# Performance work log

Hardware: AMD Instinct MI355X
Metric: run time of the kernel (lower is better)

The kernel has to match this reference:

```python
import jax, jax.numpy as jnp
import numpy as np

B, T = 64, 256
IN, HID, OUT = 512, 1024, 256
NUM_DOMAINS = 20

def setup_inputs() -> dict:
    key = jax.random.key(0)
    k1, k2, k3, k4 = jax.random.split(key, 4)
    x = jax.random.normal(k1, (B, T, IN), dtype=jnp.float32)
    hetero_info = jax.random.randint(k2, (B, 2), 0, NUM_DOMAINS, dtype=jnp.int64)
    # embedding tables init N(0, 0.02) as in the torch module
    fc1_table = 0.02 * jax.random.normal(k3, (NUM_DOMAINS, IN * HID + HID), dtype=jnp.float32)
    fc2_table = 0.02 * jax.random.normal(k4, (NUM_DOMAINS, HID * OUT + OUT), dtype=jnp.float32)
    return {"x": x, "hetero_info": hetero_info, "fc1_table": fc1_table, "fc2_table": fc2_table}

def reference(x, hetero_info, fc1_table, fc2_table):
    domain_id = hetero_info[:, 0].astype(jnp.int32)
    Bn = domain_id.shape[0]
    fc1_param = fc1_table[domain_id]                     # (B, IN*HID + HID)
    w1 = fc1_param[:, : IN * HID].reshape(Bn, IN, HID)   # (B, IN, HID)
    b1 = fc1_param[:, IN * HID:].reshape(Bn, 1, HID)
    fc2_param = fc2_table[domain_id]                     # (B, HID*OUT + OUT)
    w2 = fc2_param[:, : HID * OUT].reshape(Bn, HID, OUT) # (B, HID, OUT)
    b2 = fc2_param[:, HID * OUT:].reshape(Bn, 1, OUT)
    h = jnp.einsum('bti,bih->bth', x, w1) + b1
    h = jax.nn.gelu(h, approximate=False)  # torch nn.GELU default = exact erf
    out = jnp.einsum('bth,bho->bto', h, w2) + b2
    return out
```

## Files before the change

kernel.cpp:

```cpp
#include <hip/hip_runtime.h>
#include <math.h>

#define B_  64
#define T_  256
#define IN_ 512
#define HID_ 1024
#define OUT_ 256
#define NDOM 20

typedef __bf16 bf16_t;
typedef __bf16 bf16x8 __attribute__((ext_vector_type(8)));
typedef float  f32x4  __attribute__((ext_vector_type(4)));

__device__ __forceinline__ unsigned f2bf_bits(float f) {
    unsigned u = __builtin_bit_cast(unsigned, f);
    return (u + 0x7FFFu + ((u >> 16) & 1u)) >> 16;
}
__device__ __forceinline__ unsigned pack_bf16x2(float x, float y) {
    return f2bf_bits(x) | (f2bf_bits(y) << 16);
}

__device__ __forceinline__ void gl_lds16(const void* g, void* l) {
    __builtin_amdgcn_global_load_lds(
        (const __attribute__((address_space(1))) unsigned*)g,
        (__attribute__((address_space(3))) unsigned*)l,
        16, 0, 0);
}

__global__ __launch_bounds__(256) void prepass(
    const float* __restrict__ X,  bf16_t* __restrict__ Xbf,
    const float* __restrict__ t1, bf16_t* __restrict__ W1t, float* __restrict__ b1,
    const float* __restrict__ t2, bf16_t* __restrict__ W2t, float* __restrict__ b2)
{
    const int bid = blockIdx.x;
    const int tid = threadIdx.x;

    if (bid < 8192) {
        const size_t idx = (size_t)bid * 256 + tid;
        float4 v = ((const float4*)X)[idx];
        uint2 p;
        p.x = pack_bf16x2(v.x, v.y);
        p.y = pack_bf16x2(v.z, v.w);
        ((uint2*)Xbf)[idx] = p;
        return;
    }

    __shared__ float t[64][65];

    const float* table; bf16_t* Wt; float* Bias;
    int K, N, d, n0, k0;
    if (bid < 10752) {
        const int r = bid - 8192;
        K = IN_; N = HID_;
        d = r >> 7;
        n0 = (r & 15) * 64;
        k0 = ((r >> 4) & 7) * 64;
        table = t1; Wt = W1t; Bias = b1;
    } else {
        const int r = bid - 10752;
        K = HID_; N = OUT_;
        d = r >> 6;
        n0 = (r & 3) * 64;
        k0 = ((r >> 2) & 15) * 64;
        table = t2; Wt = W2t; Bias = b2;
    }

    const float* W = table + (size_t)d * ((size_t)K * N + N);

    #pragma unroll
    for (int r = 0; r < 4; ++r) {
        const int kl = (tid >> 4) + r * 16;
        const int nl = (tid & 15) * 4;
        float4 v = *(const float4*)(W + (size_t)(k0 + kl) * N + n0 + nl);
        t[kl][nl + 0] = v.x; t[kl][nl + 1] = v.y;
        t[kl][nl + 2] = v.z; t[kl][nl + 3] = v.w;
    }
    __syncthreads();

    bf16_t* Wtd = Wt + (size_t)d * K * N;
    #pragma unroll
    for (int r = 0; r < 4; ++r) {
        const int nl = (tid >> 4) + r * 16;
        const int k4 = (tid & 15) * 4;
        uint2 p;
        p.x = pack_bf16x2(t[k4 + 0][nl], t[k4 + 1][nl]);
        p.y = pack_bf16x2(t[k4 + 2][nl], t[k4 + 3][nl]);
        *(uint2*)(Wtd + (size_t)(n0 + nl) * K + k0 + k4) = p;
    }

    if (k0 == 0 && tid < 64)
        Bias[(size_t)d * N + n0 + tid] = W[(size_t)K * N + n0 + tid];
}

#define CT_STRIDE 136
__global__ __launch_bounds__(256) void fc1_gemm(
    const bf16_t* __restrict__ Xbf,
    const bf16_t* __restrict__ W1t,
    const float*  __restrict__ Bias,
    const int*    __restrict__ hetero,
    bf16_t*       __restrict__ H)
{
    const int id   = blockIdx.x;
    const int g    = id & 127;
    const int nidx = id >> 7;
    const int b    = g >> 1;
    const int m0   = (g & 1) * 128;
    const int n0   = nidx * 128;
    const int d    = hetero[2 * b];
    const bf16_t* W    = W1t + (size_t)d * HID_ * IN_;
    const float*  bias = Bias + (size_t)d * HID_;
    const bf16_t* A    = Xbf + (size_t)(b * 256 + m0) * IN_;

    __shared__ __attribute__((aligned(16))) char smem[128 * CT_STRIDE * 2];
    bf16_t* LdsA = (bf16_t*)smem;
    bf16_t* LdsB = (bf16_t*)(smem + 16384);
    bf16_t* Ct   = (bf16_t*)smem;

    const int tid  = threadIdx.x;
    const int wave = tid >> 6;
    const int lane = tid & 63;
    const int l16  = lane & 15;
    const int quad = lane >> 4;
    const int wm   = (wave >> 1) * 64;
    const int wn   = (wave & 1) * 64;

    f32x4 acc[4][4] = {};

    for (int kk = 0; kk < IN_; kk += 64) {
        #pragma unroll
        for (int cc = 0; cc < 4; ++cc) {
            const int r0  = wave * 32 + cc * 8;
            const int row = r0 + (lane >> 3);
            const int cs  = (lane & 7) ^ (row & 7);
            gl_lds16(A + (size_t)row * IN_ + kk + cs * 8, &LdsA[r0 * 64]);
        }
        #pragma unroll
        for (int cc = 0; cc < 4; ++cc) {
            const int r0  = wave * 32 + cc * 8;
            const int row = r0 + (lane >> 3);
            const int cs  = (lane & 7) ^ (row & 7);
            gl_lds16(W + (size_t)(n0 + row) * IN_ + kk + cs * 8, &LdsB[r0 * 64]);
        }
        __syncthreads();

        #pragma unroll
        for (int h = 0; h < 2; ++h) {
            bf16x8 af[4], bfg[4];
            #pragma unroll
            for (int i = 0; i < 4; ++i) {
                const int r = wm + i * 16 + l16;
                const int c = (h * 4 + quad) ^ (r & 7);
                af[i] = *(const bf16x8*)&LdsA[r * 64 + c * 8];
            }
            #pragma unroll
            for (int j = 0; j < 4; ++j) {
                const int r = wn + j * 16 + l16;
                const int c = (h * 4 + quad) ^ (r & 7);
                bfg[j] = *(const bf16x8*)&LdsB[r * 64 + c * 8];
            }
            #pragma unroll
            for (int i = 0; i < 4; ++i)
                #pragma unroll
                for (int j = 0; j < 4; ++j)
                    acc[i][j] = __builtin_amdgcn_mfma_f32_16x16x32_bf16(bfg[j], af[i], acc[i][j], 0, 0, 0);
        }
        __syncthreads();
    }

    #pragma unroll
    for (int i = 0; i < 4; ++i) {
        const int m = wm + i * 16 + l16;
        #pragma unroll
        for (int j = 0; j < 4; ++j) {
            const int nl = wn + j * 16 + quad * 4;
            const float4 b4 = *(const float4*)&bias[n0 + nl];
            float v0 = acc[i][j][0] + b4.x;
            float v1 = acc[i][j][1] + b4.y;
            float v2 = acc[i][j][2] + b4.z;
            float v3 = acc[i][j][3] + b4.w;
            v0 = 0.5f * v0 * (1.0f + erff(v0 * 0.70710678f));
            v1 = 0.5f * v1 * (1.0f + erff(v1 * 0.70710678f));
            v2 = 0.5f * v2 * (1.0f + erff(v2 * 0.70710678f));
            v3 = 0.5f * v3 * (1.0f + erff(v3 * 0.70710678f));
            uint2 p;
            p.x = pack_bf16x2(v0, v1);
            p.y = pack_bf16x2(v2, v3);
            *(uint2*)&Ct[m * CT_STRIDE + nl] = p;
        }
    }
    __syncthreads();

    #pragma unroll
    for (int it = 0; it < 8; ++it) {
        const int row = it * 16 + (tid >> 4);
        const int ch  = tid & 15;
        uint4 v = *(const uint4*)&Ct[row * CT_STRIDE + ch * 8];
        *(uint4*)&H[((size_t)(b * 256 + m0 + row)) * HID_ + n0 + ch * 8] = v;
    }
}

__global__ __launch_bounds__(256) void fc2_gemm(
    const bf16_t* __restrict__ H,
    const bf16_t* __restrict__ W2t,
    const float*  __restrict__ Bias,
    const int*    __restrict__ hetero,
    float*        __restrict__ Out)
{
    const int id   = blockIdx.x;
    const int g    = id & 255;
    const int nidx = id >> 8;
    const int b    = g >> 2;
    const int m0   = (g & 3) * 64;
    const int n0   = nidx * 64;
    const int d    = hetero[2 * b];
    const bf16_t* W    = W2t + (size_t)d * OUT_ * HID_;
    const float*  bias = Bias + (size_t)d * OUT_;

    __shared__ __attribute__((aligned(16))) bf16_t LdsA[64 * 128];
    __shared__ __attribute__((aligned(16))) bf16_t LdsB[64 * 128];

    const int tid  = threadIdx.x;
    const int wave = tid >> 6;
    const int lane = tid & 63;
    const int l16  = lane & 15;
    const int quad = lane >> 4;
    const int wm   = (wave >> 1) * 32;
    const int wn   = (wave & 1) * 32;

    f32x4 acc[2][2] = {};

    for (int kk = 0; kk < HID_; kk += 128) {
        #pragma unroll
        for (int cc = 0; cc < 4; ++cc) {
            const int r0  = wave * 16 + cc * 4;
            const int row = r0 + (lane >> 4);
            const int cs  = (lane & 15) ^ (row & 15);
            gl_lds16(H + (size_t)(b * 256 + m0 + row) * HID_ + kk + cs * 8,
                     &LdsA[r0 * 128]);
        }
        #pragma unroll
        for (int cc = 0; cc < 4; ++cc) {
            const int r0  = wave * 16 + cc * 4;
            const int row = r0 + (lane >> 4);
            const int cs  = (lane & 15) ^ (row & 15);
            gl_lds16(W + (size_t)(n0 + row) * HID_ + kk + cs * 8,
                     &LdsB[r0 * 128]);
        }
        __syncthreads();

        #pragma unroll
        for (int h = 0; h < 4; ++h) {
            bf16x8 af[2], bfg[2];
            #pragma unroll
            for (int i = 0; i < 2; ++i) {
                const int r = wm + i * 16 + l16;
                const int c = (h * 4 + quad) ^ (r & 15);
                af[i] = *(const bf16x8*)&LdsA[r * 128 + c * 8];
            }
            #pragma unroll
            for (int j = 0; j < 2; ++j) {
                const int r = wn + j * 16 + l16;
                const int c = (h * 4 + quad) ^ (r & 15);
                bfg[j] = *(const bf16x8*)&LdsB[r * 128 + c * 8];
            }
            #pragma unroll
            for (int i = 0; i < 2; ++i)
                #pragma unroll
                for (int j = 0; j < 2; ++j)
                    acc[i][j] = __builtin_amdgcn_mfma_f32_16x16x32_bf16(bfg[j], af[i], acc[i][j], 0, 0, 0);
        }
        __syncthreads();
    }

    #pragma unroll
    for (int i = 0; i < 2; ++i) {
        const int m = m0 + wm + i * 16 + l16;
        #pragma unroll
        for (int j = 0; j < 2; ++j) {
            const int nl = wn + j * 16 + quad * 4;
            const float4 b4 = *(const float4*)&bias[n0 + nl];
            float4 o;
            o.x = acc[i][j][0] + b4.x;
            o.y = acc[i][j][1] + b4.y;
            o.z = acc[i][j][2] + b4.z;
            o.w = acc[i][j][3] + b4.w;
            *(float4*)&Out[(size_t)(b * 256 + m) * OUT_ + n0 + nl] = o;
        }
    }
}

extern "C" void kernel_launch(void* const* d_in, const int* in_sizes, int n_in,
                              void* d_out, int out_size, void* d_ws, size_t ws_size,
                              hipStream_t stream) {
    const float* x         = (const float*)d_in[0];
    const int*   hetero    = (const int*)d_in[1];
    const float* fc1_table = (const float*)d_in[2];
    const float* fc2_table = (const float*)d_in[3];
    float*       out       = (float*)d_out;

    char* ws = (char*)d_ws;
    bf16_t* W1t = (bf16_t*)(ws);
    bf16_t* W2t = (bf16_t*)(ws + 20971520);
    float*  b1  = (float*)(ws + 31457280);
    float*  b2  = (float*)(ws + 31539200);
    bf16_t* H   = (bf16_t*)(ws + 31559680);

    bf16_t* Xbf = (bf16_t*)d_out;

    prepass<<<dim3(12032), 256, 0, stream>>>(
        x, Xbf, fc1_table, W1t, b1, fc2_table, W2t, b2);

    fc1_gemm<<<dim3(1024), 256, 0, stream>>>(Xbf, W1t, b1, hetero, H);
    fc2_gemm<<<dim3(1024), 256, 0, stream>>>(H, W2t, b2, hetero, out);
}
```

Before: 189.5 us.

## Load weights directly from global into registers and double-buffer activation tiles

Both GEMMs stop staging the weight tile through LDS. Each wave now reads its B fragments straight from global memory (L2-resident per-domain weights), and only the activation tile is staged, double-buffered so the next chunk's load overlaps the MFMAs. Tile shapes change: fc1 uses 64x256 tiles with the blocks of each batch spread across the grid, and fc2 uses 32x256 full-N tiles in 512 blocks. This removes LDS traffic and one barrier per iteration, but exposes global load latency on the weight fragments and cuts the fc2 grid size.

Result: slower. 211.4 us (+11.5%).

```diff
diff --git a/kernel.cpp b/kernel.cpp
--- a/kernel.cpp
+++ b/kernel.cpp
@@ -92,7 +92,7 @@
         Bias[(size_t)d * N + n0 + tid] = W[(size_t)K * N + n0 + tid];
 }
 
-#define CT_STRIDE 136
+#define CT1_STRIDE 264
 __global__ __launch_bounds__(256) void fc1_gemm(
     const bf16_t* __restrict__ Xbf,
     const bf16_t* __restrict__ W1t,
@@ -101,75 +101,89 @@
     bf16_t*       __restrict__ H)
 {
     const int id   = blockIdx.x;
-    const int g    = id & 127;
-    const int nidx = id >> 7;
-    const int b    = g >> 1;
-    const int m0   = (g & 1) * 128;
-    const int n0   = nidx * 128;
+    const int b    = id & 63;
+    const int rest = id >> 6;
+    const int m0   = (rest & 3) * 64;
+    const int n0   = (rest >> 2) * 256;
     const int d    = hetero[2 * b];
     const bf16_t* W    = W1t + (size_t)d * HID_ * IN_;
     const float*  bias = Bias + (size_t)d * HID_;
     const bf16_t* A    = Xbf + (size_t)(b * 256 + m0) * IN_;
 
-    __shared__ __attribute__((aligned(16))) char smem[128 * CT_STRIDE * 2];
-    bf16_t* LdsA = (bf16_t*)smem;
-    bf16_t* LdsB = (bf16_t*)(smem + 16384);
-    bf16_t* Ct   = (bf16_t*)smem;
+    __shared__ __attribute__((aligned(16))) char smem[64 * CT1_STRIDE * 2];
+    bf16_t* LdsA0 = (bf16_t*)smem;
+    bf16_t* LdsA1 = (bf16_t*)(smem + 8192);
+    bf16_t* Ct    = (bf16_t*)smem;
 
     const int tid  = threadIdx.x;
     const int wave = tid >> 6;
     const int lane = tid & 63;
     const int l16  = lane & 15;
     const int quad = lane >> 4;
-    const int wm   = (wave >> 1) * 64;
-    const int wn   = (wave & 1) * 64;
+    const int wn   = wave * 64;
+
+    const int st_r0a = wave * 16;
+    const int st_row = lane >> 3;
+    const int st_c   = lane & 7;
 
     f32x4 acc[4][4] = {};
 
-    for (int kk = 0; kk < IN_; kk += 64) {
-        #pragma unroll
-        for (int cc = 0; cc < 4; ++cc) {
-            const int r0  = wave * 32 + cc * 8;
-            const int row = r0 + (lane >> 3);
-            const int cs  = (lane & 7) ^ (row & 7);
-            gl_lds16(A + (size_t)row * IN_ + kk + cs * 8, &LdsA[r0 * 64]);
-        }
-        #pragma unroll
-        for (int cc = 0; cc < 4; ++cc) {
-            const int r0  = wave * 32 + cc * 8;
-            const int row = r0 + (lane >> 3);
-            const int cs  = (lane & 7) ^ (row & 7);
-            gl_lds16(W + (size_t)(n0 + row) * IN_ + kk + cs * 8, &LdsB[r0 * 64]);
-        }
+    {
+        bf16_t* dst = LdsA0;
+        #pragma unroll
+        for (int cc = 0; cc < 2; ++cc) {
+            const int r0  = st_r0a + cc * 8;
+            const int row = r0 + st_row;
+            const int cs  = st_c ^ (row & 7);
+            gl_lds16(A + (size_t)row * IN_ + cs * 8, &dst[r0 * 64]);
+        }
+    }
+
+    for (int kki = 0; kki < 8; ++kki) {
+        const int kk = kki * 64;
         __syncthreads();
 
+        bf16_t* cur = (kki & 1) ? LdsA1 : LdsA0;
+        if (kki < 7) {
+            bf16_t* nxt = (kki & 1) ? LdsA0 : LdsA1;
+            #pragma unroll
+            for (int cc = 0; cc < 2; ++cc) {
+                const int r0  = st_r0a + cc * 8;
+                const int row = r0 + st_row;
+                const int cs  = st_c ^ (row & 7);
+                gl_lds16(A + (size_t)row * IN_ + kk + 64 + cs * 8, &nxt[r0 * 64]);
+            }
+        }
+
+        bf16x8 bfg[2][4];
+        #pragma unroll
+        for (int h = 0; h < 2; ++h)
+            #pragma unroll
+            for (int j = 0; j < 4; ++j)
+                bfg[h][j] = *(const bf16x8*)(W +
+                    (size_t)(n0 + wn + j * 16 + l16) * IN_ + kk + h * 32 + quad * 8);
+
         #pragma unroll
         for (int h = 0; h < 2; ++h) {
-            bf16x8 af[4], bfg[4];
+            bf16x8 af[4];
             #pragma unroll
             for (int i = 0; i < 4; ++i) {
-                const int r = wm + i * 16 + l16;
+                const int r = i * 16 + l16;
                 const int c = (h * 4 + quad) ^ (r & 7);
-                af[i] = *(const bf16x8*)&LdsA[r * 64 + c * 8];
-            }
-            #pragma unroll
-            for (int j = 0; j < 4; ++j) {
-                const int r = wn + j * 16 + l16;
-                const int c = (h * 4 + quad) ^ (r & 7);
-                bfg[j] = *(const bf16x8*)&LdsB[r * 64 + c * 8];
+                af[i] = *(const bf16x8*)&cur[r * 64 + c * 8];
             }
             #pragma unroll
             for (int i = 0; i < 4; ++i)
                 #pragma unroll
                 for (int j = 0; j < 4; ++j)
-                    acc[i][j] = __builtin_amdgcn_mfma_f32_16x16x32_bf16(bfg[j], af[i], acc[i][j], 0, 0, 0);
-        }
-        __syncthreads();
-    }
+                    acc[i][j] = __builtin_amdgcn_mfma_f32_16x16x32_bf16(bfg[h][j], af[i], acc[i][j], 0, 0, 0);
+        }
+    }
+    __syncthreads();
 
     #pragma unroll
     for (int i = 0; i < 4; ++i) {
-        const int m = wm + i * 16 + l16;
+        const int m = i * 16 + l16;
         #pragma unroll
         for (int j = 0; j < 4; ++j) {
             const int nl = wn + j * 16 + quad * 4;
@@ -185,16 +199,16 @@
             uint2 p;
             p.x = pack_bf16x2(v0, v1);
             p.y = pack_bf16x2(v2, v3);
-            *(uint2*)&Ct[m * CT_STRIDE + nl] = p;
+            *(uint2*)&Ct[m * CT1_STRIDE + nl] = p;
         }
     }
     __syncthreads();
 
     #pragma unroll
     for (int it = 0; it < 8; ++it) {
-        const int row = it * 16 + (tid >> 4);
-        const int ch  = tid & 15;
-        uint4 v = *(const uint4*)&Ct[row * CT_STRIDE + ch * 8];
+        const int row = it * 8 + (tid >> 5);
+        const int ch  = tid & 31;
+        uint4 v = *(const uint4*)&Ct[row * CT1_STRIDE + ch * 8];
         *(uint4*)&H[((size_t)(b * 256 + m0 + row)) * HID_ + n0 + ch * 8] = v;
     }
 }
@@ -207,84 +221,84 @@
     float*        __restrict__ Out)
 {
     const int id   = blockIdx.x;
-    const int g    = id & 255;
-    const int nidx = id >> 8;
-    const int b    = g >> 2;
-    const int m0   = (g & 3) * 64;
-    const int n0   = nidx * 64;
+    const int b    = id & 63;
+    const int m0   = (id >> 6) * 32;
     const int d    = hetero[2 * b];
     const bf16_t* W    = W2t + (size_t)d * OUT_ * HID_;
     const float*  bias = Bias + (size_t)d * OUT_;
-
-    __shared__ __attribute__((aligned(16))) bf16_t LdsA[64 * 128];
-    __shared__ __attribute__((aligned(16))) bf16_t LdsB[64 * 128];
+    const bf16_t* A    = H + (size_t)(b * 256 + m0) * HID_;
+
+    __shared__ __attribute__((aligned(16))) bf16_t LdsA[2][32 * 64];
 
     const int tid  = threadIdx.x;
     const int wave = tid >> 6;
     const int lane = tid & 63;
     const int l16  = lane & 15;
     const int quad = lane >> 4;
-    const int wm   = (wave >> 1) * 32;
-    const int wn   = (wave & 1) * 32;
-
-    f32x4 acc[2][2] = {};
-
-    for (int kk = 0; kk < HID_; kk += 128) {
-        #pragma unroll
-        for (int cc = 0; cc < 4; ++cc) {
-            const int r0  = wave * 16 + cc * 4;
-            const int row = r0 + (lane >> 4);
-            const int cs  = (lane & 15) ^ (row & 15);
-            gl_lds16(H + (size_t)(b * 256 + m0 + row) * HID_ + kk + cs * 8,
-                     &LdsA[r0 * 128]);
-        }
-        #pragma unroll
-        for (int cc = 0; cc < 4; ++cc) {
-            const int r0  = wave * 16 + cc * 4;
-            const int row = r0 + (lane >> 4);
-            const int cs  = (lane & 15) ^ (row & 15);
-            gl_lds16(W + (size_t)(n0 + row) * HID_ + kk + cs * 8,
-                     &LdsB[r0 * 128]);
-        }
+    const int wn   = wave * 64;
+
+    const int st_r0  = wave * 8;
+    const int st_row = lane >> 3;
+    const int st_c   = lane & 7;
+
+    f32x4 acc[2][4] = {};
+
+    {
+        const int row = st_r0 + st_row;
+        const int cs  = st_c ^ (row & 7);
+        gl_lds16(A + (size_t)row * HID_ + cs * 8, &LdsA[0][st_r0 * 64]);
+    }
+
+    for (int kki = 0; kki < 16; ++kki) {
+        const int kk = kki * 64;
         __syncthreads();
 
-        #pragma unroll
-        for (int h = 0; h < 4; ++h) {
-            bf16x8 af[2], bfg[2];
+        const bf16_t* cur = LdsA[kki & 1];
+        if (kki < 15) {
+            bf16_t* nxt = LdsA[(kki + 1) & 1];
+            const int row = st_r0 + st_row;
+            const int cs  = st_c ^ (row & 7);
+            gl_lds16(A + (size_t)row * HID_ + kk + 64 + cs * 8, &nxt[st_r0 * 64]);
+        }
+
+        bf16x8 bfg[2][4];
+        #pragma unroll
+        for (int h = 0; h < 2; ++h)
+            #pragma unroll
+            for (int j = 0; j < 4; ++j)
+                bfg[h][j] = *(const bf16x8*)(W +
+                    (size_t)(wn + j * 16 + l16) * HID_ + kk + h * 32 + quad * 8);
+
+        #pragma unroll
+        for (int h = 0; h < 2; ++h) {
+            bf16x8 af[2];
             #pragma unroll
             for (int i = 0; i < 2; ++i) {
-                const int r = wm + i * 16 + l16;
-                const int c = (h * 4 + quad) ^ (r & 15);
-                af[i] = *(const bf16x8*)&LdsA[r * 128 + c * 8];
-            }
-            #pragma unroll
-            for (int j = 0; j < 2; ++j) {
-                const int r = wn + j * 16 + l16;
-                const int c = (h * 4 + quad) ^ (r & 15);
-                bfg[j] = *(const bf16x8*)&LdsB[r * 128 + c * 8];
+                const int r = i * 16 + l16;
+                const int c = (h * 4 + quad) ^ (r & 7);
+                af[i] = *(const bf16x8*)&cur[r * 64 + c * 8];
             }
             #pragma unroll
             for (int i = 0; i < 2; ++i)
                 #pragma unroll
-                for (int j = 0; j < 2; ++j)
-                    acc[i][j] = __builtin_amdgcn_mfma_f32_16x16x32_bf16(bfg[j], af[i], acc[i][j], 0, 0, 0);
-        }
-        __syncthreads();
+                for (int j = 0; j < 4; ++j)
+                    acc[i][j] = __builtin_amdgcn_mfma_f32_16x16x32_bf16(bfg[h][j], af[i], acc[i][j], 0, 0, 0);
+        }
     }
 
     #pragma unroll
     for (int i = 0; i < 2; ++i) {
-        const int m = m0 + wm + i * 16 + l16;
-        #pragma unroll
-        for (int j = 0; j < 2; ++j) {
+        const int m = m0 + i * 16 + l16;
+        #pragma unroll
+        for (int j = 0; j < 4; ++j) {
             const int nl = wn + j * 16 + quad * 4;
-            const float4 b4 = *(const float4*)&bias[n0 + nl];
+            const float4 b4 = *(const float4*)&bias[nl];
             float4 o;
             o.x = acc[i][j][0] + b4.x;
             o.y = acc[i][j][1] + b4.y;
             o.z = acc[i][j][2] + b4.z;
             o.w = acc[i][j][3] + b4.w;
-            *(float4*)&Out[(size_t)(b * 256 + m) * OUT_ + n0 + nl] = o;
+            *(float4*)&Out[(size_t)(b * 256 + m) * OUT_ + nl] = o;
         }
     }
 }
@@ -311,5 +325,5 @@
         x, Xbf, fc1_table, W1t, b1, fc2_table, W2t, b2);
 
     fc1_gemm<<<dim3(1024), 256, 0, stream>>>(Xbf, W1t, b1, hetero, H);
-    fc2_gemm<<<dim3(1024), 256, 0, stream>>>(H, W2t, b2, hetero, out);
-}
+    fc2_gemm<<<dim3(512), 256, 0, stream>>>(H, W2t, b2, hetero, out);
+}
```

## Widen fc1 GEMM tile to 128x256 and reorder block-to-batch mapping

Applied to the files above, without the earlier changes.

The fc1 GEMM block tile grows from 128x128 to 128x256, so each wave holds a 64x128 accumulator and the grid is halved to 512 blocks. Block indices now map batch fastest, and the epilogue writes the tile back in two 128-column halves through the shared staging buffer. The aim is to reuse each A tile across more output columns and cut global and LDS loads per MFMA. The cost is roughly double the accumulator registers, which may lower occupancy, and fewer blocks to spread across the CUs.

After: 249.3 us. 1.32x slower.

```diff
diff --git a/kernel.cpp b/kernel.cpp
--- a/kernel.cpp
+++ b/kernel.cpp
@@ -101,17 +101,16 @@
     bf16_t*       __restrict__ H)
 {
     const int id   = blockIdx.x;
-    const int g    = id & 127;
-    const int nidx = id >> 7;
-    const int b    = g >> 1;
-    const int m0   = (g & 1) * 128;
-    const int n0   = nidx * 128;
+    const int b    = id & 63;
+    const int rest = id >> 6;
+    const int m0   = (rest & 1) * 128;
+    const int n0   = (rest >> 1) * 256;
     const int d    = hetero[2 * b];
     const bf16_t* W    = W1t + (size_t)d * HID_ * IN_;
     const float*  bias = Bias + (size_t)d * HID_;
     const bf16_t* A    = Xbf + (size_t)(b * 256 + m0) * IN_;
 
-    __shared__ __attribute__((aligned(16))) char smem[128 * CT_STRIDE * 2];
+    __shared__ __attribute__((aligned(16))) char smem[49152];
     bf16_t* LdsA = (bf16_t*)smem;
     bf16_t* LdsB = (bf16_t*)(smem + 16384);
     bf16_t* Ct   = (bf16_t*)smem;
@@ -122,21 +121,21 @@
     const int l16  = lane & 15;
     const int quad = lane >> 4;
     const int wm   = (wave >> 1) * 64;
-    const int wn   = (wave & 1) * 64;
-
-    f32x4 acc[4][4] = {};
+    const int wn   = (wave & 1) * 128;
+
+    f32x4 acc[4][8] = {};
 
     for (int kk = 0; kk < IN_; kk += 64) {
         #pragma unroll
         for (int cc = 0; cc < 4; ++cc) {
-            const int r0  = wave * 32 + cc * 8;
+            const int r0  = cc * 32 + wave * 8;
             const int row = r0 + (lane >> 3);
             const int cs  = (lane & 7) ^ (row & 7);
             gl_lds16(A + (size_t)row * IN_ + kk + cs * 8, &LdsA[r0 * 64]);
         }
         #pragma unroll
-        for (int cc = 0; cc < 4; ++cc) {
-            const int r0  = wave * 32 + cc * 8;
+        for (int cc = 0; cc < 8; ++cc) {
+            const int r0  = cc * 32 + wave * 8;
             const int row = r0 + (lane >> 3);
             const int cs  = (lane & 7) ^ (row & 7);
             gl_lds16(W + (size_t)(n0 + row) * IN_ + kk + cs * 8, &LdsB[r0 * 64]);
@@ -145,7 +144,7 @@
 
         #pragma unroll
         for (int h = 0; h < 2; ++h) {
-            bf16x8 af[4], bfg[4];
+            bf16x8 af[4], bfg[8];
             #pragma unroll
             for (int i = 0; i < 4; ++i) {
                 const int r = wm + i * 16 + l16;
@@ -153,7 +152,7 @@
                 af[i] = *(const bf16x8*)&LdsA[r * 64 + c * 8];
             }
             #pragma unroll
-            for (int j = 0; j < 4; ++j) {
+            for (int j = 0; j < 8; ++j) {
                 const int r = wn + j * 16 + l16;
                 const int c = (h * 4 + quad) ^ (r & 7);
                 bfg[j] = *(const bf16x8*)&LdsB[r * 64 + c * 8];
@@ -161,41 +160,46 @@
             #pragma unroll
             for (int i = 0; i < 4; ++i)
                 #pragma unroll
-                for (int j = 0; j < 4; ++j)
+                for (int j = 0; j < 8; ++j)
                     acc[i][j] = __builtin_amdgcn_mfma_f32_16x16x32_bf16(bfg[j], af[i], acc[i][j], 0, 0, 0);
         }
         __syncthreads();
     }
 
     #pragma unroll
-    for (int i = 0; i < 4; ++i) {
-        const int m = wm + i * 16 + l16;
-        #pragma unroll
-        for (int j = 0; j < 4; ++j) {
-            const int nl = wn + j * 16 + quad * 4;
-            const float4 b4 = *(const float4*)&bias[n0 + nl];
-            float v0 = acc[i][j][0] + b4.x;
-            float v1 = acc[i][j][1] + b4.y;
-            float v2 = acc[i][j][2] + b4.z;
-            float v3 = acc[i][j][3] + b4.w;
-            v0 = 0.5f * v0 * (1.0f + erff(v0 * 0.70710678f));
-            v1 = 0.5f * v1 * (1.0f + erff(v1 * 0.70710678f));
-            v2 = 0.5f * v2 * (1.0f + erff(v2 * 0.70710678f));
-            v3 = 0.5f * v3 * (1.0f + erff(v3 * 0.70710678f));
-            uint2 p;
-            p.x = pack_bf16x2(v0, v1);
-            p.y = pack_bf16x2(v2, v3);
-            *(uint2*)&Ct[m * CT_STRIDE + nl] = p;
-        }
-    }
-    __syncthreads();
-
-    #pragma unroll
-    for (int it = 0; it < 8; ++it) {
-        const int row = it * 16 + (tid >> 4);
-        const int ch  = tid & 15;
-        uint4 v = *(const uint4*)&Ct[row * CT_STRIDE + ch * 8];
-        *(uint4*)&H[((size_t)(b * 256 + m0 + row)) * HID_ + n0 + ch * 8] = v;
+    for (int p = 0; p < 2; ++p) {
+        if ((wave & 1) == p) {
+            #pragma unroll
+            for (int i = 0; i < 4; ++i) {
+                const int m = wm + i * 16 + l16;
+                #pragma unroll
+                for (int j = 0; j < 8; ++j) {
+                    const int nl = j * 16 + quad * 4;
+                    const float4 b4 = *(const float4*)&bias[n0 + p * 128 + nl];
+                    float v0 = acc[i][j][0] + b4.x;
+                    float v1 = acc[i][j][1] + b4.y;
+                    float v2 = acc[i][j][2] + b4.z;
+                    float v3 = acc[i][j][3] + b4.w;
+                    v0 = 0.5f * v0 * (1.0f + erff(v0 * 0.70710678f));
+                    v1 = 0.5f * v1 * (1.0f + erff(v1 * 0.70710678f));
+                    v2 = 0.5f * v2 * (1.0f + erff(v2 * 0.70710678f));
+                    v3 = 0.5f * v3 * (1.0f + erff(v3 * 0.70710678f));
+                    uint2 pk;
+                    pk.x = pack_bf16x2(v0, v1);
+                    pk.y = pack_bf16x2(v2, v3);
+                    *(uint2*)&Ct[m * CT_STRIDE + nl] = pk;
+                }
+            }
+        }
+        __syncthreads();
+        #pragma unroll
+        for (int it = 0; it < 8; ++it) {
+            const int row = it * 16 + (tid >> 4);
+            const int ch  = tid & 15;
+            uint4 v = *(const uint4*)&Ct[row * CT_STRIDE + ch * 8];
+            *(uint4*)&H[((size_t)(b * 256 + m0 + row)) * HID_ + n0 + p * 128 + ch * 8] = v;
+        }
+        __syncthreads();
     }
 }
 
@@ -310,6 +314,6 @@
     prepass<<<dim3(12032), 256, 0, stream>>>(
         x, Xbf, fc1_table, W1t, b1, fc2_table, W2t, b2);
 
-    fc1_gemm<<<dim3(1024), 256, 0, stream>>>(Xbf, W1t, b1, hetero, H);
+    fc1_gemm<<<dim3(512), 256, 0, stream>>>(Xbf, W1t, b1, hetero, H);
     fc2_gemm<<<dim3(1024), 256, 0, stream>>>(H, W2t, b2, hetero, out);
 }
```
